# Performance work log

Measured on AMD Instinct MI355X. Metric: run time of the kernel, lower is better.

## Reference

```python
import jax, jax.numpy as jnp
import numpy as np

MSE_WEIGHT = 1.0
PHYSICS_WEIGHT = 0.1
VAR_IDX = np.array([2, 1, 0, 3, 4])
VAR_W = np.array([0.5, 0.15, 0.15, 0.1, 0.1], dtype=np.float32)
TEMP_IDX = np.array([5, 7, 8, 9, 11])
TEMP_W = 0.1
TEMP_THRESH = 5.0


def setup_inputs() -> dict:
    key = jax.random.key(0)
    k1, k2, k3, k4, k5 = jax.random.split(key, 5)
    B, S, W, D = 524288, 4, 8, 16
    return {
        "pred": jax.random.normal(k1, (B, S, D), dtype=jnp.float32),
        "target": jax.random.normal(k2, (B, S, D), dtype=jnp.float32),
        "input_sequence": jax.random.normal(k3, (B, W, D), dtype=jnp.float32),
        "scale": jax.random.uniform(k4, (D,), dtype=jnp.float32, minval=0.5, maxval=2.0),
        "mean": jax.random.normal(k5, (D,), dtype=jnp.float32),
    }


def reference(pred, target, input_sequence, scale, mean):
    B, S, D = pred.shape
    # step weights: 1/(k+1), normalized
    step_w = 1.0 / (jnp.arange(S, dtype=jnp.float32) + 1.0)
    step_w = step_w / jnp.sum(step_w)

    # --- weighted per-variable MSE (gradients flow through pred/target) ---
    var_idx = jnp.asarray(VAR_IDX)
    var_w = jnp.asarray(VAR_W)
    diff2 = (pred[:, :, var_idx] - target[:, :, var_idx]) ** 2  # [B, S, 5]
    mse_per_step = jnp.einsum("bsv,v->s", diff2, var_w) / B      # [S]
    mse_loss = jnp.dot(step_w, mse_per_step)

    # --- physics terms on detached, de-normalized states ---
    pred_sg = jax.lax.stop_gradient(pred)
    prev = jnp.concatenate(
        [jax.lax.stop_gradient(input_sequence[:, -1:, :]), pred_sg[:, :-1, :]], axis=1
    )  # [B, S, D]
    pd = pred_sg * scale + mean   # inverse_transform (StandardScaler)
    pv = prev * scale + mean

    air, water = pd[:, :, 3], pd[:, :, 4]
    heat_balance = jnp.mean((air - water) ** 2, axis=0) / (jnp.mean(air ** 2, axis=0) + 1e-6)  # [S]

    frost_dec = jax.nn.relu(pv[:, :, 2] - pd[:, :, 2])
    frost_mono = jnp.mean(frost_dec ** 2, axis=0)  # [S]

    press_dec = jax.nn.relu(pv[:, :, 0] - pd[:, :, 0]) * 0.5
    press_growth = jnp.mean(press_dec ** 2, axis=0)  # [S]

    tidx = jnp.asarray(TEMP_IDX)
    temp_diff = jnp.abs(pd[:, :, tidx] - pv[:, :, tidx])            # [B, S, 5]
    temp_pen = TEMP_W * jnp.sum(jnp.mean(jax.nn.relu(temp_diff - TEMP_THRESH) ** 2, axis=0), axis=-1)  # [S]

    physics_per_step = heat_balance + frost_mono + press_growth + temp_pen  # [S]
    physics_loss = jnp.dot(step_w, physics_per_step)

    return MSE_WEIGHT * mse_loss + PHYSICS_WEIGHT * physics_loss
```

## Files before the change

### kernel.cpp

```cpp
#include <hip/hip_runtime.h>

#define B_TOTAL 524288
#define TILE_B 128
#define NBLK (B_TOTAL / TILE_B)
#define NTHR 512


__global__ __launch_bounds__(NTHR, 8) void loss_partial(
    const float* __restrict__ pred,
    const float* __restrict__ target,
    const float* __restrict__ inseq,
    const float* __restrict__ scale,
    const float* __restrict__ mean,
    float* __restrict__ partials)
{
    __shared__ float4 sp[TILE_B * 12];
    __shared__ float4 st[TILE_B * 8];

    const int tid = threadIdx.x;
    const size_t tile0 = (size_t)blockIdx.x * TILE_B;

    const float4* prg = reinterpret_cast<const float4*>(pred) + tile0 * 16;
    const float4* tgg = reinterpret_cast<const float4*>(target) + tile0 * 16;

#pragma unroll
    for (int it = 0; it < 3; ++it) {
        int j = it * NTHR + tid;
        int row = j / 3, k = j - row * 3;
        sp[j ^ ((j >> 3) & 7)] = prg[row * 4 + k];
    }
#pragma unroll
    for (int it = 0; it < 2; ++it) {
        int j = it * NTHR + tid;
        st[j ^ ((j >> 3) & 7)] = tgg[((j >> 1) << 2) | (j & 1)];
    }

    const int b = tid >> 2;
    const int s = tid & 3;

    float pv0 = 0.f, pv2 = 0.f, pv5 = 0.f, pv7 = 0.f, pv8 = 0.f, pv9 = 0.f, pv11 = 0.f;
    if (s == 0) {
        const float4* iq = reinterpret_cast<const float4*>(inseq + (tile0 + (size_t)b) * 128 + 112);
        float4 q0 = iq[0], q1 = iq[1], q2 = iq[2];
        pv0 = q0.x; pv2 = q0.z; pv5 = q1.y; pv7 = q1.w;
        pv8 = q2.x; pv9 = q2.y; pv11 = q2.w;
    }

    const float sc0 = scale[0], sc2 = scale[2], sc3 = scale[3], sc4 = scale[4];
    const float sc5 = scale[5], sc7 = scale[7], sc8 = scale[8], sc9 = scale[9], sc11 = scale[11];
    const float mn3 = mean[3], mn4 = mean[4];
    const float sw = (s == 0) ? 0.48f : (s == 1) ? 0.24f : (s == 2) ? 0.16f : 0.12f;

    __syncthreads();

    auto ldp = [&](int row, int w) -> float4 {
        int i = row * 3 + w;
        return sp[i ^ ((i >> 3) & 7)];
    };
    auto ldt = [&](int row, int h) -> float4 {
        int i = row * 2 + h;
        return st[i ^ ((i >> 3) & 7)];
    };

    const int row = b * 4 + s;
    if (s != 0) {
        float4 q0 = ldp(row - 1, 0), q1 = ldp(row - 1, 1), q2 = ldp(row - 1, 2);
        pv0 = q0.x; pv2 = q0.z; pv5 = q1.y; pv7 = q1.w;
        pv8 = q2.x; pv9 = q2.y; pv11 = q2.w;
    }

    float4 p0 = ldp(row, 0), p1 = ldp(row, 1), p2 = ldp(row, 2);
    float4 t0 = ldt(row, 0), t1 = ldt(row, 1);

    float d0 = p0.x - t0.x, d1 = p0.y - t0.y, d2 = p0.z - t0.z;
    float d3 = p0.w - t0.w, d4 = p1.x - t1.x;
    float acc_mse = sw * (0.15f * d0 * d0 + 0.15f * d1 * d1 + 0.5f * d2 * d2 +
                          0.1f * d3 * d3 + 0.1f * d4 * d4);

    float air = p0.w * sc3 + mn3;
    float water = p1.x * sc4 + mn4;
    float hdf = air - water;
    float hn = hdf * hdf;
    float hd = air * air;

    float fr = fmaxf((pv2 - p0.z) * sc2, 0.f);
    float pg = fmaxf((pv0 - p0.x) * sc0, 0.f) * 0.5f;
    float rest = fr * fr + pg * pg;
    float t5 = fmaxf(fabsf(p1.y - pv5) * sc5 - 5.f, 0.f);
    float t7 = fmaxf(fabsf(p1.w - pv7) * sc7 - 5.f, 0.f);
    float t8 = fmaxf(fabsf(p2.x - pv8) * sc8 - 5.f, 0.f);
    float t9 = fmaxf(fabsf(p2.y - pv9) * sc9 - 5.f, 0.f);
    float t11 = fmaxf(fabsf(p2.w - pv11) * sc11 - 5.f, 0.f);
    rest += 0.1f * (t5 * t5 + t7 * t7 + t8 * t8 + t9 * t9 + t11 * t11);
    float acc_rest = sw * rest;

    __syncthreads();

    const int lane = tid & 63;
    const int wave = tid >> 6;
#pragma unroll
    for (int off = 1; off < 64; off <<= 1) {
        acc_mse  += __shfl_xor(acc_mse, off, 64);
        acc_rest += __shfl_xor(acc_rest, off, 64);
    }
#pragma unroll
    for (int off = 4; off < 64; off <<= 1) {
        hn += __shfl_xor(hn, off, 64);
        hd += __shfl_xor(hd, off, 64);
    }

    float* red = reinterpret_cast<float*>(st);
    if (lane == 0) { red[wave * 10 + 0] = acc_mse; red[wave * 10 + 1] = acc_rest; }
    if (lane < 4)  { red[wave * 10 + 2 + lane] = hn; red[wave * 10 + 6 + lane] = hd; }
    __syncthreads();

    if (tid < 10) {
        float v = 0.f;
#pragma unroll
        for (int w = 0; w < 8; ++w) v += red[w * 10 + tid];
        partials[tid * NBLK + blockIdx.x] = v;
    }
}

__global__ __launch_bounds__(640) void loss_final(
    const float* __restrict__ partials,
    float* __restrict__ out)
{
    __shared__ float tot[10];
    const int t = threadIdx.x;
    const int c = t >> 6;
    const int lane = t & 63;

    float v = 0.f;
#pragma unroll
    for (int i = 0; i < NBLK / 64; ++i)
        v += partials[(size_t)c * NBLK + i * 64 + lane];
#pragma unroll
    for (int off = 32; off; off >>= 1) v += __shfl_down(v, off, 64);
    if (lane == 0) tot[c] = v;
    __syncthreads();

    if (t == 0) {
        const float stepw[4] = {0.48f, 0.24f, 0.16f, 0.12f};
        const float invB = 1.0f / (float)B_TOTAL;
        float mse = tot[0] * invB;
        float phys = tot[1] * invB;
#pragma unroll
        for (int s = 0; s < 4; ++s) {
            float num = tot[2 + s] * invB;
            float den = tot[6 + s] * invB + 1e-6f;
            phys += stepw[s] * (num / den);
        }
        out[0] = mse + 0.1f * phys;
    }
}

extern "C" void kernel_launch(void* const* d_in, const int* in_sizes, int n_in,
                              void* d_out, int out_size, void* d_ws, size_t ws_size,
                              hipStream_t stream) {
    const float* pred   = (const float*)d_in[0];
    const float* target = (const float*)d_in[1];
    const float* inseq  = (const float*)d_in[2];
    const float* scale  = (const float*)d_in[3];
    const float* mean   = (const float*)d_in[4];
    float* out = (float*)d_out;
    float* partials = (float*)d_ws;

    loss_partial<<<NBLK, NTHR, 0, stream>>>(pred, target, inseq, scale, mean, partials);
    loss_final<<<1, 640, 0, stream>>>(partials, out);
}
```

Baseline: 62.20 us.

## Fuse final reduction via last-block ticket and process four tiles per block

Each block now loops over four consecutive tiles, so the grid shrinks to 1024 blocks and per-block setup and reduction overhead is amortized. The separate final-reduction kernel is replaced by an atomic ticket counter: the last block to finish reads all partials and writes the output. This removes a second kernel launch but adds a memset launch, fences and atomics. Per-tile loads are serialized behind two barriers each iteration, which can reduce memory-level parallelism.

```diff
diff --git a/kernel.cpp b/kernel.cpp
--- a/kernel.cpp
+++ b/kernel.cpp
@@ -2,99 +2,106 @@
 
 #define B_TOTAL 524288
 #define TILE_B 128
-#define NBLK (B_TOTAL / TILE_B)
+#define TPB 4
+#define GRID (B_TOTAL / (TILE_B * TPB))
 #define NTHR 512
 
 
-__global__ __launch_bounds__(NTHR, 8) void loss_partial(
+__global__ __launch_bounds__(NTHR, 8) void loss_fused(
     const float* __restrict__ pred,
     const float* __restrict__ target,
     const float* __restrict__ inseq,
     const float* __restrict__ scale,
     const float* __restrict__ mean,
-    float* __restrict__ partials)
+    float* __restrict__ partials,
+    int* __restrict__ counter,
+    float* __restrict__ out)
 {
     __shared__ float4 sp[TILE_B * 12];
     __shared__ float4 st[TILE_B * 8];
+    float* sf = reinterpret_cast<float*>(st);
 
     const int tid = threadIdx.x;
-    const size_t tile0 = (size_t)blockIdx.x * TILE_B;
-
-    const float4* prg = reinterpret_cast<const float4*>(pred) + tile0 * 16;
-    const float4* tgg = reinterpret_cast<const float4*>(target) + tile0 * 16;
-
-#pragma unroll
-    for (int it = 0; it < 3; ++it) {
-        int j = it * NTHR + tid;
-        int row = j / 3, k = j - row * 3;
-        sp[j ^ ((j >> 3) & 7)] = prg[row * 4 + k];
-    }
-#pragma unroll
-    for (int it = 0; it < 2; ++it) {
-        int j = it * NTHR + tid;
-        st[j ^ ((j >> 3) & 7)] = tgg[((j >> 1) << 2) | (j & 1)];
-    }
-
     const int b = tid >> 2;
     const int s = tid & 3;
-
-    float pv0 = 0.f, pv2 = 0.f, pv5 = 0.f, pv7 = 0.f, pv8 = 0.f, pv9 = 0.f, pv11 = 0.f;
-    if (s == 0) {
-        const float4* iq = reinterpret_cast<const float4*>(inseq + (tile0 + (size_t)b) * 128 + 112);
-        float4 q0 = iq[0], q1 = iq[1], q2 = iq[2];
-        pv0 = q0.x; pv2 = q0.z; pv5 = q1.y; pv7 = q1.w;
-        pv8 = q2.x; pv9 = q2.y; pv11 = q2.w;
-    }
+    const int row = tid;
 
     const float sc0 = scale[0], sc2 = scale[2], sc3 = scale[3], sc4 = scale[4];
     const float sc5 = scale[5], sc7 = scale[7], sc8 = scale[8], sc9 = scale[9], sc11 = scale[11];
     const float mn3 = mean[3], mn4 = mean[4];
     const float sw = (s == 0) ? 0.48f : (s == 1) ? 0.24f : (s == 2) ? 0.16f : 0.12f;
 
-    __syncthreads();
-
-    auto ldp = [&](int row, int w) -> float4 {
-        int i = row * 3 + w;
+    auto ldp = [&](int r, int w) -> float4 {
+        int i = r * 3 + w;
         return sp[i ^ ((i >> 3) & 7)];
     };
-    auto ldt = [&](int row, int h) -> float4 {
-        int i = row * 2 + h;
+    auto ldt = [&](int r, int h) -> float4 {
+        int i = r * 2 + h;
         return st[i ^ ((i >> 3) & 7)];
     };
 
-    const int row = b * 4 + s;
-    if (s != 0) {
-        float4 q0 = ldp(row - 1, 0), q1 = ldp(row - 1, 1), q2 = ldp(row - 1, 2);
-        pv0 = q0.x; pv2 = q0.z; pv5 = q1.y; pv7 = q1.w;
-        pv8 = q2.x; pv9 = q2.y; pv11 = q2.w;
+    float acc_mse = 0.f, acc_rest = 0.f, hn = 0.f, hd = 0.f;
+
+    for (int t = 0; t < TPB; ++t) {
+        const size_t tile0 = ((size_t)blockIdx.x * TPB + t) * TILE_B;
+        const float4* prg = reinterpret_cast<const float4*>(pred) + tile0 * 16;
+        const float4* tgg = reinterpret_cast<const float4*>(target) + tile0 * 16;
+
+#pragma unroll
+        for (int it = 0; it < 3; ++it) {
+            int j = it * NTHR + tid;
+            int r2 = j / 3, k = j - r2 * 3;
+            sp[j ^ ((j >> 3) & 7)] = prg[r2 * 4 + k];
+        }
+#pragma unroll
+        for (int it = 0; it < 2; ++it) {
+            int j = it * NTHR + tid;
+            st[j ^ ((j >> 3) & 7)] = tgg[((j >> 1) << 2) | (j & 1)];
+        }
+
+        float pv0 = 0.f, pv2 = 0.f, pv5 = 0.f, pv7 = 0.f, pv8 = 0.f, pv9 = 0.f, pv11 = 0.f;
+        if (s == 0) {
+            const float4* iq = reinterpret_cast<const float4*>(inseq) + (tile0 + (size_t)b) * 32 + 28;
+            float4 q0 = iq[0], q1 = iq[1], q2 = iq[2];
+            pv0 = q0.x; pv2 = q0.z; pv5 = q1.y; pv7 = q1.w;
+            pv8 = q2.x; pv9 = q2.y; pv11 = q2.w;
+        }
+
+        __syncthreads();
+
+        if (s != 0) {
+            float4 q0 = ldp(row - 1, 0), q1 = ldp(row - 1, 1), q2 = ldp(row - 1, 2);
+            pv0 = q0.x; pv2 = q0.z; pv5 = q1.y; pv7 = q1.w;
+            pv8 = q2.x; pv9 = q2.y; pv11 = q2.w;
+        }
+
+        float4 p0 = ldp(row, 0), p1 = ldp(row, 1), p2 = ldp(row, 2);
+        float4 t0 = ldt(row, 0), t1 = ldt(row, 1);
+
+        float d0 = p0.x - t0.x, d1 = p0.y - t0.y, d2 = p0.z - t0.z;
+        float d3 = p0.w - t0.w, d4 = p1.x - t1.x;
+        acc_mse += sw * (0.15f * d0 * d0 + 0.15f * d1 * d1 + 0.5f * d2 * d2 +
+                         0.1f * d3 * d3 + 0.1f * d4 * d4);
+
+        float air = p0.w * sc3 + mn3;
+        float water = p1.x * sc4 + mn4;
+        float hdf = air - water;
+        hn += hdf * hdf;
+        hd += air * air;
+
+        float fr = fmaxf((pv2 - p0.z) * sc2, 0.f);
+        float pg = fmaxf((pv0 - p0.x) * sc0, 0.f) * 0.5f;
+        float rest = fr * fr + pg * pg;
+        float t5 = fmaxf(fabsf(p1.y - pv5) * sc5 - 5.f, 0.f);
+        float t7 = fmaxf(fabsf(p1.w - pv7) * sc7 - 5.f, 0.f);
+        float t8 = fmaxf(fabsf(p2.x - pv8) * sc8 - 5.f, 0.f);
+        float t9 = fmaxf(fabsf(p2.y - pv9) * sc9 - 5.f, 0.f);
+        float t11 = fmaxf(fabsf(p2.w - pv11) * sc11 - 5.f, 0.f);
+        rest += 0.1f * (t5 * t5 + t7 * t7 + t8 * t8 + t9 * t9 + t11 * t11);
+        acc_rest += sw * rest;
+
+        __syncthreads();
     }
-
-    float4 p0 = ldp(row, 0), p1 = ldp(row, 1), p2 = ldp(row, 2);
-    float4 t0 = ldt(row, 0), t1 = ldt(row, 1);
-
-    float d0 = p0.x - t0.x, d1 = p0.y - t0.y, d2 = p0.z - t0.z;
-    float d3 = p0.w - t0.w, d4 = p1.x - t1.x;
-    float acc_mse = sw * (0.15f * d0 * d0 + 0.15f * d1 * d1 + 0.5f * d2 * d2 +
-                          0.1f * d3 * d3 + 0.1f * d4 * d4);
-
-    float air = p0.w * sc3 + mn3;
-    float water = p1.x * sc4 + mn4;
-    float hdf = air - water;
-    float hn = hdf * hdf;
-    float hd = air * air;
-
-    float fr = fmaxf((pv2 - p0.z) * sc2, 0.f);
-    float pg = fmaxf((pv0 - p0.x) * sc0, 0.f) * 0.5f;
-    float rest = fr * fr + pg * pg;
-    float t5 = fmaxf(fabsf(p1.y - pv5) * sc5 - 5.f, 0.f);
-    float t7 = fmaxf(fabsf(p1.w - pv7) * sc7 - 5.f, 0.f);
-    float t8 = fmaxf(fabsf(p2.x - pv8) * sc8 - 5.f, 0.f);
-    float t9 = fmaxf(fabsf(p2.y - pv9) * sc9 - 5.f, 0.f);
-    float t11 = fmaxf(fabsf(p2.w - pv11) * sc11 - 5.f, 0.f);
-    rest += 0.1f * (t5 * t5 + t7 * t7 + t8 * t8 + t9 * t9 + t11 * t11);
-    float acc_rest = sw * rest;
-
-    __syncthreads();
 
     const int lane = tid & 63;
     const int wave = tid >> 6;
@@ -108,48 +115,58 @@
         hn += __shfl_xor(hn, off, 64);
         hd += __shfl_xor(hd, off, 64);
     }
-
-    float* red = reinterpret_cast<float*>(st);
-    if (lane == 0) { red[wave * 10 + 0] = acc_mse; red[wave * 10 + 1] = acc_rest; }
-    if (lane < 4)  { red[wave * 10 + 2 + lane] = hn; red[wave * 10 + 6 + lane] = hd; }
+    if (lane == 0) { sf[wave * 10 + 0] = acc_mse; sf[wave * 10 + 1] = acc_rest; }
+    if (lane < 4)  { sf[wave * 10 + 2 + lane] = hn; sf[wave * 10 + 6 + lane] = hd; }
     __syncthreads();
 
     if (tid < 10) {
         float v = 0.f;
 #pragma unroll
-        for (int w = 0; w < 8; ++w) v += red[w * 10 + tid];
-        partials[tid * NBLK + blockIdx.x] = v;
+        for (int w = 0; w < 8; ++w) v += sf[w * 10 + tid];
+        __hip_atomic_store(&partials[tid * GRID + blockIdx.x], v,
+                           __ATOMIC_RELAXED, __HIP_MEMORY_SCOPE_AGENT);
+        __threadfence();
     }
-}
-
-__global__ __launch_bounds__(640) void loss_final(
-    const float* __restrict__ partials,
-    float* __restrict__ out)
-{
-    __shared__ float tot[10];
-    const int t = threadIdx.x;
-    const int c = t >> 6;
-    const int lane = t & 63;
-
-    float v = 0.f;
-#pragma unroll
-    for (int i = 0; i < NBLK / 64; ++i)
-        v += partials[(size_t)c * NBLK + i * 64 + lane];
-#pragma unroll
-    for (int off = 32; off; off >>= 1) v += __shfl_down(v, off, 64);
-    if (lane == 0) tot[c] = v;
     __syncthreads();
 
-    if (t == 0) {
+    if (tid == 0) {
+        int ticket = atomicAdd(counter, 1);
+        ((int*)sf)[104] = (ticket == GRID - 1);
+    }
+    __syncthreads();
+    if (!((int*)sf)[104]) return;
+
+    __threadfence();
+    float* tot = sf + 80;
+    float* red2 = sf + 96;
+    for (int c = 0; c < 10; ++c) {
+        float v = __hip_atomic_load(&partials[c * GRID + tid],
+                                    __ATOMIC_RELAXED, __HIP_MEMORY_SCOPE_AGENT)
+                + __hip_atomic_load(&partials[c * GRID + 512 + tid],
+                                    __ATOMIC_RELAXED, __HIP_MEMORY_SCOPE_AGENT);
+#pragma unroll
+        for (int off = 32; off; off >>= 1) v += __shfl_down(v, off, 64);
+        if (lane == 0) red2[wave] = v;
+        __syncthreads();
+        if (tid == 0) {
+            float u = 0.f;
+#pragma unroll
+            for (int w = 0; w < 8; ++w) u += red2[w];
+            tot[c] = u;
+        }
+        __syncthreads();
+    }
+
+    if (tid == 0) {
         const float stepw[4] = {0.48f, 0.24f, 0.16f, 0.12f};
         const float invB = 1.0f / (float)B_TOTAL;
         float mse = tot[0] * invB;
         float phys = tot[1] * invB;
 #pragma unroll
-        for (int s = 0; s < 4; ++s) {
-            float num = tot[2 + s] * invB;
-            float den = tot[6 + s] * invB + 1e-6f;
-            phys += stepw[s] * (num / den);
+        for (int q = 0; q < 4; ++q) {
+            float num = tot[2 + q] * invB;
+            float den = tot[6 + q] * invB + 1e-6f;
+            phys += stepw[q] * (num / den);
         }
         out[0] = mse + 0.1f * phys;
     }
@@ -165,7 +182,9 @@
     const float* mean   = (const float*)d_in[4];
     float* out = (float*)d_out;
     float* partials = (float*)d_ws;
+    int* counter = (int*)((char*)d_ws + 10 * GRID * sizeof(float));
 
-    loss_partial<<<NBLK, NTHR, 0, stream>>>(pred, target, inseq, scale, mean, partials);
-    loss_final<<<1, 640, 0, stream>>>(partials, out);
+    hipMemsetAsync(counter, 0, sizeof(int), stream);
+    loss_fused<<<GRID, NTHR, 0, stream>>>(pred, target, inseq, scale, mean,
+                                          partials, counter, out);
 }
```

New measurement: 130.0 us. 2.09x slower.
